# Optimization experiments

Hardware: AMD Instinct MI355X
Metric: run time of the kernel (lower is better)

Reference implementation:

```python
import jax, jax.numpy as jnp
import numpy as np

B, N, D = 64, 784, 768
H, HD, G = 32, 24, 2
HID = 3072
SCALE = HD ** -0.5
EPS = 1e-6


def _ln(x, g, b):
    m = jnp.mean(x, -1, keepdims=True)
    v = jnp.mean((x - m) ** 2, -1, keepdims=True)
    return (x - m) * jax.lax.rsqrt(v + EPS) * g + b


def setup_inputs() -> dict:
    key = jax.random.key(0)
    ks = jax.random.split(key, 12)
    def rn(k, shape, s=0.02):
        return (jax.random.normal(k, shape) * s).astype(jnp.float32)
    return {
        'x_cls': jax.random.normal(ks[0], (B, 1, D), jnp.float32),
        'x_img': jax.random.normal(ks[1], (B, N, D), jnp.float32),
        'ln1_g': jnp.ones((D,), jnp.float32), 'ln1_b': jnp.zeros((D,), jnp.float32),
        'Wq': rn(ks[2], (D, D)), 'bq': jnp.zeros((D,), jnp.float32),
        'Wk': rn(ks[3], (D, D)), 'bk': jnp.zeros((D,), jnp.float32),
        'Wv': rn(ks[4], (D, D)), 'bv': jnp.zeros((D,), jnp.float32),
        'w1_W': rn(ks[5], (H, H), 0.1), 'w1_b': jnp.zeros((H,), jnp.float32),
        'w2_W': rn(ks[6], (H, H), 0.1), 'w2_b': jnp.zeros((H,), jnp.float32),
        'proj_W': rn(ks[7], (D, D)), 'proj_b': jnp.zeros((D,), jnp.float32),
        'ln2_g': jnp.ones((D,), jnp.float32), 'ln2_b': jnp.zeros((D,), jnp.float32),
        'fc1_W': rn(ks[8], (G, HID // G, D // G)), 'fc1_b': jnp.zeros((G, HID // G), jnp.float32),
        'fc2_W': rn(ks[9], (G, D // G, HID // G)), 'fc2_b': jnp.zeros((G, D // G), jnp.float32),
    }


def reference(x_cls, x_img, ln1_g, ln1_b, Wq, bq, Wk, bk, Wv, bv,
              w1_W, w1_b, w2_W, w2_b, proj_W, proj_b, ln2_g, ln2_b,
              fc1_W, fc1_b, fc2_W, fc2_b):
    # --- ClassAttention (non-mismatch path), dropout = identity (eval) ---
    u = jnp.concatenate([x_cls, x_img], axis=1)  # [B, M, D], M = N+1
    M = u.shape[1]
    n = _ln(u, ln1_g, ln1_b)
    q = ((n[:, :1] @ Wq + bq).reshape(B, 1, H, HD).transpose(0, 2, 1, 3)) * SCALE  # [B,H,1,HD]
    k = (n @ Wk + bk).reshape(B, M, H, HD).transpose(0, 2, 1, 3)                   # [B,H,M,HD]
    v = (n @ Wv + bv).reshape(B, M, H, HD).transpose(0, 2, 1, 3)
    attn = jnp.einsum('bhqd,bhkd->bhqk', q, k)  # [B,H,1,M]
    # interactive score mixing across heads (w1 pre-softmax, w2 post-softmax)
    attn = attn + jnp.einsum('bhqk,hg->bgqk', attn, w1_W) + w1_b[None, :, None, None]
    attn = jax.nn.softmax(attn, axis=-1)
    attn = attn + jnp.einsum('bhqk,hg->bgqk', attn, w2_W) + w2_b[None, :, None, None]
    o = jnp.einsum('bhqk,bhkd->bhqd', attn, v).transpose(0, 2, 1, 3).reshape(B, 1, D)
    x_cls = x_cls + (o @ proj_W + proj_b)
    # --- GroupConvMlp on the cls token (grouped 1x1 convs + channel shuffle) ---
    y = _ln(x_cls, ln2_g, ln2_b)
    h = jnp.einsum('btgc,goc->btgo', y.reshape(B, 1, G, D // G), fc1_W) + fc1_b  # group-major out channels
    h = jax.nn.gelu(h.reshape(B, 1, HID), approximate=False)
    # channel_shuffle(group=G): out channel b*gc+a = in channel a*G+b
    h = h.reshape(B, 1, HID // G, G).transpose(0, 1, 3, 2).reshape(B, 1, HID)
    z = jnp.einsum('btgc,goc->btgo', h.reshape(B, 1, G, HID // G), fc2_W) + fc2_b
    x_cls = x_cls + z.reshape(B, 1, D)
    return (x_cls, x_img)
```

## Files before the change

### kernel.cpp

```cpp
#include <hip/hip_runtime.h>
#include <hip/hip_bf16.h>
#include <math.h>

#define BB   64
#define NN   784
#define DD   768
#define HH   32
#define HD24 24
#define MM   785
#define HIDN 3072
#define QSCALE 0.20412414523193154f
#define LNEPS 1e-6f

#define WS_Q     0
#define WS_RS    49152
#define WS_RM    100352
#define WS_S1P   151552
#define WS_BQP   163840
#define WS_LMX   176128
#define WS_LSM   184320
#define WS_A2P   192512
#define WS_WMP   200704
#define WS_PS    208896
#define WS_C1    210432
#define WS_H2    259584
#define WS_O     456192
#define WS_E     505344
#define WS_T     2143744
#define WS_ZP    0

__device__ __forceinline__ unsigned packbf(float a, float b) {
  union { __hip_bfloat162 h2; unsigned u; } cv;
  cv.h2 = __float22bfloat162_rn(make_float2(a, b));
  return cv.u;
}
__device__ __forceinline__ float lo16(unsigned w) { return __uint_as_float(w << 16); }
__device__ __forceinline__ float hi16(unsigned w) { return __uint_as_float(w & 0xffff0000u); }

__global__ __launch_bounds__(256) void k_q(
    const float* __restrict__ x_cls,
    const float* __restrict__ g1, const float* __restrict__ b1,
    const float* __restrict__ Wq, const float* __restrict__ bq,
    float* __restrict__ ws)
{
  const int b = blockIdx.y;
  const int oc0 = blockIdx.x * 64;
  const int t = threadIdx.x;
  const int lane = t & 63, wid = t >> 6;

  __shared__ __align__(16) float nc_l[DD];
  __shared__ float red4[4][64];
  __shared__ float rS[4], rQ[4];
  __shared__ float musd[2];

  float xv[3];
  float s = 0.f, q2 = 0.f;
#pragma unroll
  for (int k = 0; k < 3; ++k) {
    float v = x_cls[(size_t)b * DD + t + 256 * k];
    xv[k] = v; s += v; q2 += v * v;
  }
#pragma unroll
  for (int off = 1; off < 64; off <<= 1) { s += __shfl_xor(s, off); q2 += __shfl_xor(q2, off); }
  if (lane == 0) { rS[wid] = s; rQ[wid] = q2; }
  __syncthreads();
  if (t == 0) {
    float ss = rS[0] + rS[1] + rS[2] + rS[3];
    float qq = rQ[0] + rQ[1] + rQ[2] + rQ[3];
    float mu = ss * (1.f / DD);
    musd[0] = mu; musd[1] = rsqrtf(qq * (1.f / DD) - mu * mu + LNEPS);
  }
  __syncthreads();
  {
    float mu = musd[0], rs = musd[1];
#pragma unroll
    for (int k = 0; k < 3; ++k) {
      int d = t + 256 * k;
      nc_l[d] = (xv[k] - mu) * rs * g1[d] + b1[d];
    }
  }
  __syncthreads();

  const int oc = t & 63, ks = t >> 6;
  const float* wp = Wq + (size_t)(ks * 192) * DD + oc0 + oc;
  const float* ncp = nc_l + ks * 192;
  float a0 = 0.f, a1 = 0.f, a2 = 0.f, a3 = 0.f;
#pragma unroll 4
  for (int d = 0; d < 192; d += 4) {
    a0 += ncp[d + 0] * wp[(size_t)(d + 0) * DD];
    a1 += ncp[d + 1] * wp[(size_t)(d + 1) * DD];
    a2 += ncp[d + 2] * wp[(size_t)(d + 2) * DD];
    a3 += ncp[d + 3] * wp[(size_t)(d + 3) * DD];
  }
  red4[ks][oc] = (a0 + a1) + (a2 + a3);
  __syncthreads();
  if (t < 64) {
    int ocg = oc0 + t;
    ws[WS_Q + (size_t)b * DD + ocg] =
        (red4[0][t] + red4[1][t] + red4[2][t] + red4[3][t] + bq[ocg]) * QSCALE;
  }
}

__global__ __launch_bounds__(256) void k_gqk(
    const float* __restrict__ g1, const float* __restrict__ b1,
    const float* __restrict__ Wk, const float* __restrict__ w1W,
    float* __restrict__ ws)
{
  const int b = blockIdx.y;
  const int d0 = blockIdx.x * 128;
  const int t = threadIdx.x;

  __shared__ __align__(16) float q_l[DD];
  __shared__ float T1[HH * HH];
  __shared__ float qk_l[128][33];
  __shared__ float pS[8][HH], pB[8][HH];

  for (int i = t; i < DD; i += 256) q_l[i] = ws[WS_Q + (size_t)b * DD + i];
  for (int i = t; i < HH * HH; i += 256) {
    int g = i >> 5, h = i & 31;
    T1[i] = w1W[i] + ((g == h) ? 1.f : 0.f);
  }
  __syncthreads();

  {
    const int dl = t >> 1, gh = t & 1;
    const float4* wr = (const float4*)(Wk + (size_t)(d0 + dl) * DD + gh * 384);
    const float4* qr = (const float4*)(q_l + gh * 384);
#pragma unroll 4
    for (int gg = 0; gg < 16; ++gg) {
      float a = 0.f;
#pragma unroll
      for (int c = 0; c < 6; ++c) {
        float4 w = wr[gg * 6 + c];
        float4 p = qr[gg * 6 + c];
        a += w.x * p.x + w.y * p.y + w.z * p.z + w.w * p.w;
      }
      qk_l[dl][gh * 16 + gg] = a;
    }
  }
  __syncthreads();
  {
    const int h = t & 31, dg = t >> 5;
    float fb[16];
    float s1a = 0.f, bqa = 0.f;
#pragma unroll 2
    for (int dd = 0; dd < 16; ++dd) {
      int dl = dg * 16 + dd;
      float f = 0.f;
#pragma unroll 8
      for (int g = 0; g < HH; ++g) f += qk_l[dl][g] * T1[g * HH + h];
      float gq = g1[d0 + dl] * f;
      fb[dd] = gq;
      s1a += gq;
      bqa += b1[d0 + dl] * qk_l[dl][h];
    }
    float* gout = ws + WS_E + ((size_t)b * HH + h) * DD + d0 + dg * 16;
#pragma unroll
    for (int k = 0; k < 4; ++k)
      *(float4*)(gout + k * 4) = make_float4(fb[4*k], fb[4*k+1], fb[4*k+2], fb[4*k+3]);
    pS[dg][h] = s1a; pB[dg][h] = bqa;
  }
  __syncthreads();
  if (t < HH) {
    float s = 0.f, bq = 0.f;
#pragma unroll
    for (int k = 0; k < 8; ++k) { s += pS[k][t]; bq += pB[k][t]; }
    ws[WS_S1P + ((size_t)b * 6 + blockIdx.x) * HH + t] = s;
    ws[WS_BQP + ((size_t)b * 6 + blockIdx.x) * HH + t] = bq;
  }
}

__global__ __launch_bounds__(256) void k_main1(
    const float* __restrict__ x_cls, const float* __restrict__ x_img,
    float* __restrict__ out, float* __restrict__ ws)
{
  const int b = blockIdx.y;
  const int m0 = blockIdx.x * 64;
  const int t = threadIdx.x;
  const int rp = t >> 3;
  const int pc = (t & 7) * 4;
  const int mo = t & 7;
  const int dsub = (t >> 3) & 7;
  const int th = t >> 6;

  __shared__ unsigned uT[32][36];
  __shared__ __align__(16) float gqT[32][36];

  const float* gq_src = ws + WS_E + (size_t)b * (HH * DD);
  float* out_img = out + (size_t)BB * DD;

  const int ma = m0 + 2 * rp;
  const int mb = ma + 1;
  const bool va = (ma < MM), vb = (mb < MM);
  const float* rowA = (ma == 0) ? (x_cls + (size_t)b * DD)
                                : (x_img + ((size_t)b * NN + (ma - 1)) * DD);
  const float* rowB = x_img + ((size_t)b * NN + (mb - 1)) * DD;
  float* orowA = out_img + ((size_t)b * NN + (ma - 1)) * DD;
  float* orowB = out_img + ((size_t)b * NN + (mb - 1)) * DD;

  float4 pf0, pf1, pfg;
  float sl0 = 0.f, sq0 = 0.f, sl1 = 0.f, sq1 = 0.f;

  auto LOADX = [&](int dc) {
    pf0 = va ? *(const float4*)(rowA + dc * 32 + pc) : make_float4(0.f,0.f,0.f,0.f);
    pf1 = vb ? *(const float4*)(rowB + dc * 32 + pc) : make_float4(0.f,0.f,0.f,0.f);
    sl0 += pf0.x + pf0.y + pf0.z + pf0.w;
    sq0 += pf0.x*pf0.x + pf0.y*pf0.y + pf0.z*pf0.z + pf0.w*pf0.w;
    sl1 += pf1.x + pf1.y + pf1.z + pf1.w;
    sq1 += pf1.x*pf1.x + pf1.y*pf1.y + pf1.z*pf1.z + pf1.w*pf1.w;
    pfg = *(const float4*)(gq_src + (size_t)rp * DD + dc * 32 + pc);
  };
  auto STOREX = [&](int dc) {
    if (va && ma >= 1) *(float4*)(orowA + dc * 32 + pc) = pf0;
    if (vb)            *(float4*)(orowB + dc * 32 + pc) = pf1;
    uT[pc + 0][rp] = packbf(pf0.x, pf1.x);
    uT[pc + 1][rp] = packbf(pf0.y, pf1.y);
    uT[pc + 2][rp] = packbf(pf0.z, pf1.z);
    uT[pc + 3][rp] = packbf(pf0.w, pf1.w);
    *(float4*)&gqT[rp][pc] = pfg;
  };

  float acc[8][8];
#pragma unroll
  for (int i = 0; i < 8; ++i)
#pragma unroll
    for (int j = 0; j < 8; ++j) acc[i][j] = 0.f;

  LOADX(0); STOREX(0); __syncthreads();

#define K1_DD2(COMP, DD2LIT)                                            \
  {                                                                     \
    uint4 uw = *(const uint4*)&uT[dsub * 4 + DD2LIT][mo * 4];           \
    float um0 = lo16(uw.x), um1 = hi16(uw.x);                           \
    float um2 = lo16(uw.y), um3 = hi16(uw.y);                           \
    float um4 = lo16(uw.z), um5 = hi16(uw.z);                           \
    float um6 = lo16(uw.w), um7 = hi16(uw.w);                           \
    _Pragma("unroll")                                                   \
    for (int j = 0; j < 8; ++j) {                                       \
      const float g = gq4[j].COMP;                                      \
      acc[0][j] += um0 * g; acc[1][j] += um1 * g;                       \
      acc[2][j] += um2 * g; acc[3][j] += um3 * g;                       \
      acc[4][j] += um4 * g; acc[5][j] += um5 * g;                       \
      acc[6][j] += um6 * g; acc[7][j] += um7 * g;                       \
    }                                                                   \
  }

  for (int dc = 0; dc < 24; ++dc) {
    if (dc < 23) LOADX(dc + 1);
    float4 gq4[8];
#pragma unroll
    for (int j = 0; j < 8; ++j) gq4[j] = *(const float4*)&gqT[th * 8 + j][dsub * 4];
    K1_DD2(x, 0)
    K1_DD2(y, 1)
    K1_DD2(z, 2)
    K1_DD2(w, 3)
    __syncthreads();
    if (dc < 23) STOREX(dc + 1);
    __syncthreads();
  }
#undef K1_DD2

#pragma unroll
  for (int i = 0; i < 8; ++i)
#pragma unroll
    for (int j = 0; j < 8; ++j) {
      float v = acc[i][j];
      v += __shfl_xor(v, 8);
      v += __shfl_xor(v, 16);
      v += __shfl_xor(v, 32);
      acc[i][j] = v;
    }
  if (dsub == 0) {
    float* tb = ws + WS_T + (size_t)b * MM * HH;
#pragma unroll
    for (int i = 0; i < 8; ++i) {
      int m = m0 + mo * 8 + i;
      if (m < MM) {
        float* dst = tb + (size_t)m * HH + th * 8;
        *(float4*)dst = make_float4(acc[i][0], acc[i][1], acc[i][2], acc[i][3]);
        *(float4*)(dst + 4) = make_float4(acc[i][4], acc[i][5], acc[i][6], acc[i][7]);
      }
    }
  }
#pragma unroll
  for (int off = 1; off < 8; off <<= 1) {
    sl0 += __shfl_xor(sl0, off); sq0 += __shfl_xor(sq0, off);
    sl1 += __shfl_xor(sl1, off); sq1 += __shfl_xor(sq1, off);
  }
  if ((t & 7) == 0) {
    if (va) {
      float mu = sl0 * (1.f / DD);
      float rs = rsqrtf(sq0 * (1.f / DD) - mu * mu + LNEPS);
      ws[WS_RS + (size_t)b * 800 + ma] = rs;
      ws[WS_RM + (size_t)b * 800 + ma] = rs * mu;
    }
    if (vb) {
      float mu = sl1 * (1.f / DD);
      float rs = rsqrtf(sq1 * (1.f / DD) - mu * mu + LNEPS);
      ws[WS_RS + (size_t)b * 800 + mb] = rs;
      ws[WS_RM + (size_t)b * 800 + mb] = rs * mu;
    }
  }
}

__global__ __launch_bounds__(256) void k_sm_a(
    const float* __restrict__ bk,
    const float* __restrict__ w1W, const float* __restrict__ w1b,
    float* __restrict__ ws)
{
  const int cx = blockIdx.x, b = blockIdx.y;
  const int t = threadIdx.x;
  const int lane = t & 63, wid = t >> 6;

  __shared__ float T1[HH * HH];
  __shared__ float s1_sh[HH], c0_sh[HH], bq_sh[HH];
  __shared__ float red[4][HH];
  __shared__ float lmax_sh[HH];

  for (int i = t; i < HH * HH; i += 256) {
    int g = i >> 5, h = i & 31;
    T1[i] = w1W[i] + ((g == h) ? 1.f : 0.f);
  }
  if (t < HH) {
    float s1v = 0.f, bqv = 0.f;
#pragma unroll
    for (int p = 0; p < 6; ++p) {
      s1v += ws[WS_S1P + ((size_t)b * 6 + p) * HH + t];
      bqv += ws[WS_BQP + ((size_t)b * 6 + p) * HH + t];
    }
    const float* qp = ws + WS_Q + (size_t)b * DD + t * HD24;
#pragma unroll
    for (int j = 0; j < HD24; ++j) bqv += bk[t * HD24 + j] * qp[j];
    s1_sh[t] = s1v; bq_sh[t] = bqv;
  }
  __syncthreads();
  if (t < HH) {
    float c0 = w1b[t];
#pragma unroll
    for (int g = 0; g < HH; ++g) c0 += T1[g * HH + t] * bq_sh[g];
    c0_sh[t] = c0;
  }
  __syncthreads();

  const int m = cx * 256 + t;
  const bool vm = (m < MM);
  float a1[HH];
  if (vm) {
    const float* tb = ws + WS_T + ((size_t)b * MM + m) * HH;
    float rs = ws[WS_RS + (size_t)b * 800 + m];
    float rm = ws[WS_RM + (size_t)b * 800 + m];
#pragma unroll
    for (int q = 0; q < 8; ++q) {
      float4 tv = *(const float4*)(tb + q * 4);
      a1[4*q+0] = rs * tv.x - rm * s1_sh[4*q+0] + c0_sh[4*q+0];
      a1[4*q+1] = rs * tv.y - rm * s1_sh[4*q+1] + c0_sh[4*q+1];
      a1[4*q+2] = rs * tv.z - rm * s1_sh[4*q+2] + c0_sh[4*q+2];
      a1[4*q+3] = rs * tv.w - rm * s1_sh[4*q+3] + c0_sh[4*q+3];
    }
  } else {
#pragma unroll
    for (int h = 0; h < HH; ++h) a1[h] = -3.0e38f;
  }
#pragma unroll
  for (int h = 0; h < HH; ++h) {
    float v = a1[h];
#pragma unroll
    for (int off = 1; off < 64; off <<= 1) v = fmaxf(v, __shfl_xor(v, off));
    if (lane == 0) red[wid][h] = v;
  }
  __syncthreads();
  if (t < HH) {
    float v = fmaxf(fmaxf(red[0][t], red[1][t]), fmaxf(red[2][t], red[3][t]));
    lmax_sh[t] = v;
    ws[WS_LMX + ((size_t)b * 4 + cx) * HH + t] = v;
  }
  __syncthreads();
  float* E = ws + WS_E + (size_t)b * (HH * 800);
  if (vm) {
#pragma unroll
    for (int h = 0; h < HH; ++h) {
      float e = __expf(a1[h] - lmax_sh[h]);
      a1[h] = e;
      E[(size_t)h * 800 + m] = e;
    }
  } else {
#pragma unroll
    for (int h = 0; h < HH; ++h) a1[h] = 0.f;
  }
#pragma unroll
  for (int h = 0; h < HH; ++h) {
    float v = a1[h];
#pragma unroll
    for (int off = 1; off < 64; off <<= 1) v += __shfl_xor(v, off);
    if (lane == 0) red[wid][h] = v;
  }
  __syncthreads();
  if (t < HH)
    ws[WS_LSM + ((size_t)b * 4 + cx) * HH + t] = red[0][t] + red[1][t] + red[2][t] + red[3][t];
}

__global__ __launch_bounds__(256) void k_sm_b(
    const float* __restrict__ w2W, const float* __restrict__ w2b,
    float* __restrict__ ws)
{
  const int cx = blockIdx.x, b = blockIdx.y;
  const int t = threadIdx.x;
  const int lane = t & 63, wid = t >> 6;

  __shared__ __align__(16) float T2s[HH * HH];
  __shared__ float inv_sh[HH], w2b_sh[HH];
  __shared__ float red[4][HH];

  if (t < HH) {
    float l0 = ws[WS_LMX + ((size_t)b * 4 + 0) * HH + t];
    float l1 = ws[WS_LMX + ((size_t)b * 4 + 1) * HH + t];
    float l2 = ws[WS_LMX + ((size_t)b * 4 + 2) * HH + t];
    float l3 = ws[WS_LMX + ((size_t)b * 4 + 3) * HH + t];
    float gmax = fmaxf(fmaxf(l0, l1), fmaxf(l2, l3));
    float s = ws[WS_LSM + ((size_t)b * 4 + 0) * HH + t] * __expf(l0 - gmax)
            + ws[WS_LSM + ((size_t)b * 4 + 1) * HH + t] * __expf(l1 - gmax)
            + ws[WS_LSM + ((size_t)b * 4 + 2) * HH + t] * __expf(l2 - gmax)
            + ws[WS_LSM + ((size_t)b * 4 + 3) * HH + t] * __expf(l3 - gmax);
    float lcx = (cx == 0) ? l0 : (cx == 1) ? l1 : (cx == 2) ? l2 : l3;
    inv_sh[t] = __expf(lcx - gmax) / s;
    w2b_sh[t] = w2b[t];
  }
  __syncthreads();
  for (int i = t; i < HH * HH; i += 256) {
    int g = i >> 5, h = i & 31;
    T2s[i] = (w2W[i] + ((g == h) ? 1.f : 0.f)) * inv_sh[g];
  }
  __syncthreads();

  const int m = cx * 256 + t;
  float* E = ws + WS_E + (size_t)b * (HH * 800);
  float4 av[8];
#pragma unroll
  for (int q = 0; q < 8; ++q) av[q] = make_float4(0.f,0.f,0.f,0.f);
  float rm = 0.f;
  if (m < MM) {
    float rs = ws[WS_RS + (size_t)b * 800 + m];
    rm = ws[WS_RM + (size_t)b * 800 + m];
#pragma unroll 4
    for (int g = 0; g < HH; ++g) {
      float eg = E[(size_t)g * 800 + m];
#pragma unroll
      for (int q = 0; q < 8; ++q) {
        float4 t2 = *(const float4*)&T2s[g * HH + q * 4];
        av[q].x += eg * t2.x; av[q].y += eg * t2.y;
        av[q].z += eg * t2.z; av[q].w += eg * t2.w;
      }
    }
#pragma unroll
    for (int q = 0; q < 8; ++q) {
      av[q].x += w2b_sh[q*4+0]; av[q].y += w2b_sh[q*4+1];
      av[q].z += w2b_sh[q*4+2]; av[q].w += w2b_sh[q*4+3];
      E[(size_t)(q*4+0) * 800 + m] = av[q].x * rs;
      E[(size_t)(q*4+1) * 800 + m] = av[q].y * rs;
      E[(size_t)(q*4+2) * 800 + m] = av[q].z * rs;
      E[(size_t)(q*4+3) * 800 + m] = av[q].w * rs;
    }
  } else if (m < 800) {
#pragma unroll
    for (int h = 0; h < HH; ++h) E[(size_t)h * 800 + m] = 0.f;
  }
#pragma unroll
  for (int h = 0; h < HH; ++h) {
    float v = ((const float*)&av[h >> 2])[h & 3];
#pragma unroll
    for (int off = 1; off < 64; off <<= 1) v += __shfl_xor(v, off);
    if (lane == 0) red[wid][h] = v;
  }
  __syncthreads();
  if (t < HH)
    ws[WS_A2P + ((size_t)b * 4 + cx) * HH + t] = red[0][t] + red[1][t] + red[2][t] + red[3][t];
  __syncthreads();
#pragma unroll
  for (int h = 0; h < HH; ++h) {
    float v = ((const float*)&av[h >> 2])[h & 3] * rm;
#pragma unroll
    for (int off = 1; off < 64; off <<= 1) v += __shfl_xor(v, off);
    if (lane == 0) red[wid][h] = v;
  }
  __syncthreads();
  if (t < HH)
    ws[WS_WMP + ((size_t)b * 4 + cx) * HH + t] = red[0][t] + red[1][t] + red[2][t] + red[3][t];
}

__global__ __launch_bounds__(256) void k_wsum(
    const float* __restrict__ x_cls, const float* __restrict__ x_img,
    float* __restrict__ ws)
{
  const int b = blockIdx.y;
  const int d0 = blockIdx.x * 64;
  const int t = threadIdx.x;
  const int dseg = t & 15;
  const int msub = (t >> 4) & 3;
  const int hb = (t >> 6) * 8;

  __shared__ __align__(16) float w_s[HH][36];
  const float* W = ws + WS_E + (size_t)b * (HH * 800);

  float acc[8][4];
#pragma unroll
  for (int j = 0; j < 8; ++j)
#pragma unroll
    for (int c = 0; c < 4; ++c) acc[j][c] = 0.f;

  float4 pu[8], pun[8];
  float4 pwn;

  auto LOADU = [&](int mc, float4* dst) {
#pragma unroll
    for (int i = 0; i < 8; ++i) {
      int m = mc * 32 + msub * 8 + i;
      if (m < MM) {
        const float* src = (m == 0) ? (x_cls + (size_t)b * DD)
                                    : (x_img + ((size_t)b * NN + (m - 1)) * DD);
        dst[i] = *(const float4*)(src + d0 + dseg * 4);
      } else dst[i] = make_float4(0.f,0.f,0.f,0.f);
    }
  };

  LOADU(0, pu);
  {
    float4 pw = *(const float4*)(W + (size_t)(t >> 3) * 800 + (t & 7) * 4);
    *(float4*)&w_s[t >> 3][(t & 7) * 4] = pw;
  }
  __syncthreads();

  for (int mc = 0; mc < 25; ++mc) {
    if (mc < 24) {
      pwn = *(const float4*)(W + (size_t)(t >> 3) * 800 + (mc + 1) * 32 + (t & 7) * 4);
      LOADU(mc + 1, pun);
    }
#pragma unroll
    for (int j = 0; j < 8; ++j) {
      float4 wA = *(const float4*)&w_s[hb + j][msub * 8];
      float4 wB = *(const float4*)&w_s[hb + j][msub * 8 + 4];
      float wv0 = wA.x, wv1 = wA.y, wv2 = wA.z, wv3 = wA.w;
      float wv4 = wB.x, wv5 = wB.y, wv6 = wB.z, wv7 = wB.w;
      acc[j][0] += wv0*pu[0].x + wv1*pu[1].x + wv2*pu[2].x + wv3*pu[3].x
                 + wv4*pu[4].x + wv5*pu[5].x + wv6*pu[6].x + wv7*pu[7].x;
      acc[j][1] += wv0*pu[0].y + wv1*pu[1].y + wv2*pu[2].y + wv3*pu[3].y
                 + wv4*pu[4].y + wv5*pu[5].y + wv6*pu[6].y + wv7*pu[7].y;
      acc[j][2] += wv0*pu[0].z + wv1*pu[1].z + wv2*pu[2].z + wv3*pu[3].z
                 + wv4*pu[4].z + wv5*pu[5].z + wv6*pu[6].z + wv7*pu[7].z;
      acc[j][3] += wv0*pu[0].w + wv1*pu[1].w + wv2*pu[2].w + wv3*pu[3].w
                 + wv4*pu[4].w + wv5*pu[5].w + wv6*pu[6].w + wv7*pu[7].w;
    }
    __syncthreads();
    if (mc < 24) {
      *(float4*)&w_s[t >> 3][(t & 7) * 4] = pwn;
#pragma unroll
      for (int i = 0; i < 8; ++i) pu[i] = pun[i];
    }
    __syncthreads();
  }

#pragma unroll
  for (int j = 0; j < 8; ++j)
#pragma unroll
    for (int c = 0; c < 4; ++c) {
      float v = acc[j][c];
      v += __shfl_xor(v, 16);
      v += __shfl_xor(v, 32);
      acc[j][c] = v;
    }
  if (msub == 0) {
    float* R = ws + WS_T + (size_t)b * HH * DD;
#pragma unroll
    for (int j = 0; j < 8; ++j)
      *(float4*)(R + (size_t)(hb + j) * DD + d0 + dseg * 4) =
          make_float4(acc[j][0], acc[j][1], acc[j][2], acc[j][3]);
  }
}

__global__ __launch_bounds__(192) void k_att_o(
    const float* __restrict__ g1, const float* __restrict__ b1,
    const float* __restrict__ Wv, const float* __restrict__ bv,
    float* __restrict__ ws)
{
  const int h = blockIdx.x;
  const int b = blockIdx.y;
  const int t = threadIdx.x;

  __shared__ __align__(16) float agg_l[DD];
  __shared__ float red[8][25];
  __shared__ float a2wm[2];

  if (t == 0) {
    float a = 0.f;
#pragma unroll
    for (int c = 0; c < 4; ++c) a += ws[WS_A2P + ((size_t)b * 4 + c) * HH + h];
    a2wm[0] = a;
  }
  if (t == 1) {
    float w = 0.f;
#pragma unroll
    for (int c = 0; c < 4; ++c) w += ws[WS_WMP + ((size_t)b * 4 + c) * HH + h];
    a2wm[1] = w;
  }
  __syncthreads();
  const float A2 = a2wm[0], WM = a2wm[1];
  const float* R = ws + WS_T + ((size_t)b * HH + h) * DD;
  for (int i = t; i < DD; i += 192)
    agg_l[i] = g1[i] * (R[i] - WM) + b1[i] * A2;
  __syncthreads();

  const int oc = t % 24, ks = t / 24;
  const float* wv = Wv + (size_t)(ks * 96) * DD + h * HD24 + oc;
  const float* ag = agg_l + ks * 96;
  float a0 = 0.f, a1 = 0.f, a2 = 0.f, a3 = 0.f;
#pragma unroll 4
  for (int d = 0; d < 96; d += 4) {
    a0 += ag[d + 0] * wv[(size_t)(d + 0) * DD];
    a1 += ag[d + 1] * wv[(size_t)(d + 1) * DD];
    a2 += ag[d + 2] * wv[(size_t)(d + 2) * DD];
    a3 += ag[d + 3] * wv[(size_t)(d + 3) * DD];
  }
  red[ks][oc] = (a0 + a1) + (a2 + a3);
  __syncthreads();
  if (t < 24) {
    float o = A2 * bv[h * HD24 + t];
#pragma unroll
    for (int k = 0; k < 8; ++k) o += red[k][t];
    ws[WS_O + (size_t)b * DD + h * HD24 + t] = o;
  }
}

__global__ __launch_bounds__(256) void k_proj2(
    const float* __restrict__ x_cls,
    const float* __restrict__ projW, const float* __restrict__ projb,
    float* __restrict__ ws)
{
  const int b = blockIdx.y;
  const int oc0 = blockIdx.x * 64;
  const int t = threadIdx.x;

  __shared__ __align__(16) float o_l[DD];
  __shared__ float red4[4][64];

  for (int i = t; i < DD; i += 256) o_l[i] = ws[WS_O + (size_t)b * DD + i];
  __syncthreads();

  const int oc = t & 63, ks = t >> 6;
  const float* wp = projW + (size_t)(ks * 192) * DD + oc0 + oc;
  const float* op = o_l + ks * 192;
  float a0 = 0.f, a1 = 0.f, a2 = 0.f, a3 = 0.f;
#pragma unroll 4
  for (int d = 0; d < 192; d += 4) {
    a0 += op[d + 0] * wp[(size_t)(d + 0) * DD];
    a1 += op[d + 1] * wp[(size_t)(d + 1) * DD];
    a2 += op[d + 2] * wp[(size_t)(d + 2) * DD];
    a3 += op[d + 3] * wp[(size_t)(d + 3) * DD];
  }
  red4[ks][oc] = (a0 + a1) + (a2 + a3);
  __syncthreads();
  if (t < 64) {
    int ocg = oc0 + t;
    float c1 = red4[0][t] + red4[1][t] + red4[2][t] + red4[3][t]
             + projb[ocg] + x_cls[(size_t)b * DD + ocg];
    ws[WS_C1 + (size_t)b * DD + ocg] = c1;
    float cs = c1, cq = c1 * c1;
#pragma unroll
    for (int off = 1; off < 64; off <<= 1) { cs += __shfl_xor(cs, off); cq += __shfl_xor(cq, off); }
    if (t == 0) {
      ws[WS_PS + ((size_t)b * 12 + blockIdx.x) * 2 + 0] = cs;
      ws[WS_PS + ((size_t)b * 12 + blockIdx.x) * 2 + 1] = cq;
    }
  }
}

__global__ __launch_bounds__(256) void k_fc1(
    const float* __restrict__ fc1W, const float* __restrict__ fc1b,
    const float* __restrict__ g2, const float* __restrict__ b2,
    float* __restrict__ ws)
{
  const int g = blockIdx.x / 48;
  const int oc0 = (blockIdx.x % 48) * 32;
  const int t = threadIdx.x;
  const int txo = t & 7, tyb = t >> 3;

  __shared__ float y_s[64][65];
  __shared__ float w_s[32][65];
  __shared__ float mv[64][2];

  if (t < 64) {
    float s = 0.f, q = 0.f;
#pragma unroll
    for (int p = 0; p < 12; ++p) {
      s += ws[WS_PS + ((size_t)t * 12 + p) * 2 + 0];
      q += ws[WS_PS + ((size_t)t * 12 + p) * 2 + 1];
    }
    float mu = s * (1.f / DD);
    mv[t][0] = mu;
    mv[t][1] = rsqrtf(q * (1.f / DD) - mu * mu + LNEPS);
  }
  __syncthreads();

  float acc[2][4];
#pragma unroll
  for (int i = 0; i < 2; ++i)
#pragma unroll
    for (int j = 0; j < 4; ++j) acc[i][j] = 0.f;

#pragma unroll 1
  for (int kc = 0; kc < 6; ++kc) {
    {
      int r = t >> 2;
      float mu = mv[r][0], rs = mv[r][1];
#pragma unroll
      for (int p = 0; p < 4; ++p) {
        int c = (t & 3) * 4 + p * 16;
        int gc = g * 384 + kc * 64 + c;
        float4 v = *(const float4*)(ws + WS_C1 + (size_t)r * DD + gc);
        float4 gg = *(const float4*)(g2 + gc);
        float4 bb = *(const float4*)(b2 + gc);
        y_s[r][c+0] = (v.x - mu) * rs * gg.x + bb.x;
        y_s[r][c+1] = (v.y - mu) * rs * gg.y + bb.y;
        y_s[r][c+2] = (v.z - mu) * rs * gg.z + bb.z;
        y_s[r][c+3] = (v.w - mu) * rs * gg.w + bb.w;
      }
      int rw = t >> 3;
#pragma unroll
      for (int p = 0; p < 2; ++p) {
        int c = (t & 7) * 4 + p * 32;
        float4 w = *(const float4*)(fc1W + ((size_t)(g * 1536 + oc0 + rw)) * 384 + kc * 64 + c);
        w_s[rw][c+0] = w.x; w_s[rw][c+1] = w.y; w_s[rw][c+2] = w.z; w_s[rw][c+3] = w.w;
      }
    }
    __syncthreads();
#pragma unroll 4
    for (int kk = 0; kk < 64; ++kk) {
      float y0 = y_s[2*tyb+0][kk], y1 = y_s[2*tyb+1][kk];
      float w0 = w_s[4*txo+0][kk], w1 = w_s[4*txo+1][kk];
      float w2 = w_s[4*txo+2][kk], w3 = w_s[4*txo+3][kk];
      acc[0][0] += y0*w0; acc[0][1] += y0*w1; acc[0][2] += y0*w2; acc[0][3] += y0*w3;
      acc[1][0] += y1*w0; acc[1][1] += y1*w1; acc[1][2] += y1*w2; acc[1][3] += y1*w3;
    }
    __syncthreads();
  }

  float* H2 = ws + WS_H2;
#pragma unroll
  for (int i = 0; i < 2; ++i) {
    int bb = 2 * tyb + i;
#pragma unroll
    for (int j = 0; j < 4; ++j) {
      int oc = oc0 + 4 * txo + j;
      float v = acc[i][j] + fc1b[g * 1536 + oc];
      v = 0.5f * v * (1.f + erff(v * 0.70710678118654752f));
      H2[(size_t)bb * HIDN + (oc & 1) * 1536 + g * 768 + (oc >> 1)] = v;
    }
  }
}

__global__ __launch_bounds__(256) void k_fc2(
    const float* __restrict__ fc2W, float* __restrict__ ws)
{
  const int oc0 = blockIdx.x * 32;
  const int kq = blockIdx.y;
  const int g = blockIdx.z;
  const int t = threadIdx.x;
  const int txo = t & 7, tyb = t >> 3;

  __shared__ float h_s[64][65];
  __shared__ float w_s[32][65];

  float acc[2][4];
#pragma unroll
  for (int i = 0; i < 2; ++i)
#pragma unroll
    for (int j = 0; j < 4; ++j) acc[i][j] = 0.f;

  const float* H2 = ws + WS_H2;

#pragma unroll 1
  for (int kc = 0; kc < 6; ++kc) {
    {
      int r = t >> 2;
#pragma unroll
      for (int p = 0; p < 4; ++p) {
        int c = (t & 3) * 4 + p * 16;
        float4 v = *(const float4*)(H2 + (size_t)r * HIDN + g * 1536 + kq * 384 + kc * 64 + c);
        h_s[r][c+0] = v.x; h_s[r][c+1] = v.y; h_s[r][c+2] = v.z; h_s[r][c+3] = v.w;
      }
      int rw = t >> 3;
#pragma unroll
      for (int p = 0; p < 2; ++p) {
        int c = (t & 7) * 4 + p * 32;
        float4 w = *(const float4*)(fc2W + ((size_t)(g * 384 + oc0 + rw)) * 1536 + kq * 384 + kc * 64 + c);
        w_s[rw][c+0] = w.x; w_s[rw][c+1] = w.y; w_s[rw][c+2] = w.z; w_s[rw][c+3] = w.w;
      }
    }
    __syncthreads();
#pragma unroll 4
    for (int kk = 0; kk < 64; ++kk) {
      float y0 = h_s[2*tyb+0][kk], y1 = h_s[2*tyb+1][kk];
      float w0 = w_s[4*txo+0][kk], w1 = w_s[4*txo+1][kk];
      float w2 = w_s[4*txo+2][kk], w3 = w_s[4*txo+3][kk];
      acc[0][0] += y0*w0; acc[0][1] += y0*w1; acc[0][2] += y0*w2; acc[0][3] += y0*w3;
      acc[1][0] += y1*w0; acc[1][1] += y1*w1; acc[1][2] += y1*w2; acc[1][3] += y1*w3;
    }
    __syncthreads();
  }

  float* ZP = ws + WS_ZP + (size_t)kq * BB * DD;
#pragma unroll
  for (int i = 0; i < 2; ++i)
#pragma unroll
    for (int j = 0; j < 4; ++j)
      ZP[(size_t)(2 * tyb + i) * DD + g * 384 + oc0 + 4 * txo + j] = acc[i][j];
}

__global__ __launch_bounds__(256) void k_final(
    const float* __restrict__ fc2b, float* __restrict__ out, const float* __restrict__ ws)
{
  int idx = blockIdx.x * 256 + threadIdx.x;
  int d = idx % DD;
  float v = ws[WS_C1 + idx] + fc2b[d];
#pragma unroll
  for (int kq = 0; kq < 4; ++kq) v += ws[WS_ZP + (size_t)kq * BB * DD + idx];
  out[idx] = v;
}

extern "C" void kernel_launch(void* const* d_in, const int* in_sizes, int n_in,
                              void* d_out, int out_size, void* d_ws, size_t ws_size,
                              hipStream_t stream)
{
  (void)in_sizes; (void)n_in; (void)out_size; (void)ws_size;
  const float* x_cls = (const float*)d_in[0];
  const float* x_img = (const float*)d_in[1];
  const float* ln1_g = (const float*)d_in[2];
  const float* ln1_b = (const float*)d_in[3];
  const float* Wq    = (const float*)d_in[4];
  const float* bq    = (const float*)d_in[5];
  const float* Wk    = (const float*)d_in[6];
  const float* bk    = (const float*)d_in[7];
  const float* Wv    = (const float*)d_in[8];
  const float* bv    = (const float*)d_in[9];
  const float* w1W   = (const float*)d_in[10];
  const float* w1b   = (const float*)d_in[11];
  const float* w2W   = (const float*)d_in[12];
  const float* w2b   = (const float*)d_in[13];
  const float* projW = (const float*)d_in[14];
  const float* projb = (const float*)d_in[15];
  const float* ln2_g = (const float*)d_in[16];
  const float* ln2_b = (const float*)d_in[17];
  const float* fc1W  = (const float*)d_in[18];
  const float* fc1b  = (const float*)d_in[19];
  const float* fc2W  = (const float*)d_in[20];
  const float* fc2b  = (const float*)d_in[21];
  float* out = (float*)d_out;
  float* ws  = (float*)d_ws;

  k_q    <<<dim3(12, 64), dim3(256), 0, stream>>>(x_cls, ln1_g, ln1_b, Wq, bq, ws);
  k_gqk  <<<dim3(6, 64),  dim3(256), 0, stream>>>(ln1_g, ln1_b, Wk, w1W, ws);
  k_main1<<<dim3(13, 64), dim3(256), 0, stream>>>(x_cls, x_img, out, ws);
  k_sm_a <<<dim3(4, 64),  dim3(256), 0, stream>>>(bk, w1W, w1b, ws);
  k_sm_b <<<dim3(4, 64),  dim3(256), 0, stream>>>(w2W, w2b, ws);
  k_wsum <<<dim3(12, 64), dim3(256), 0, stream>>>(x_cls, x_img, ws);
  k_att_o<<<dim3(32, 64), dim3(192), 0, stream>>>(ln1_g, ln1_b, Wv, bv, ws);
  k_proj2<<<dim3(12, 64), dim3(256), 0, stream>>>(x_cls, projW, projb, ws);
  k_fc1  <<<dim3(96),     dim3(256), 0, stream>>>(fc1W, fc1b, ln2_g, ln2_b, ws);
  k_fc2  <<<dim3(12, 4, 2), dim3(256), 0, stream>>>(fc2W, ws);
  k_final<<<dim3(192),    dim3(256), 0, stream>>>(fc2b, out, ws);
}
```

Before: 335.7 us.

## Use bf16 MFMA for the x·gq score projection with pre-swizzled B operand

The producer kernel now writes the gq matrix as bf16 in the MFMA B-operand lane layout, and k_main1 replaces its scalar FMA outer-product loop and LDS staging with 16x16x32 bf16 MFMA instructions. A-operand rows are read directly from global memory per lane, while the x_img-to-output copy is done in a separate coalesced loop. This is meant to remove the VALU-bound inner product and the shared-memory transposes and barriers. The cost is that each input row is read twice from global memory (once for the copy, once for the A operand), the gq values drop to bf16, and the A-operand reads are less coalesced.

Result: faster. 320.4 us (-4.6%).

```diff
diff --git a/kernel.cpp b/kernel.cpp
--- a/kernel.cpp
+++ b/kernel.cpp
@@ -29,6 +29,9 @@
 #define WS_T     2143744
 #define WS_ZP    0
 
+typedef __attribute__((ext_vector_type(8))) short bf16x8;
+typedef __attribute__((ext_vector_type(4))) float f32x4;
+
 __device__ __forceinline__ unsigned packbf(float a, float b) {
   union { __hip_bfloat162 h2; unsigned u; } cv;
   cv.h2 = __float22bfloat162_rn(make_float2(a, b));
@@ -154,10 +157,16 @@
       s1a += gq;
       bqa += b1[d0 + dl] * qk_l[dl][h];
     }
-    float* gout = ws + WS_E + ((size_t)b * HH + h) * DD + d0 + dg * 16;
-#pragma unroll
-    for (int k = 0; k < 4; ++k)
-      *(float4*)(gout + k * 4) = make_float4(fb[4*k], fb[4*k+1], fb[4*k+2], fb[4*k+3]);
+    const int kstep = (d0 >> 5) + (dg >> 1);
+    const int nt = h >> 4;
+    const int lane0 = (h & 15) + 32 * (dg & 1);
+    uint4* GQB = (uint4*)(ws + WS_E) + (size_t)b * (24 * 2 * 64);
+    GQB[(kstep * 2 + nt) * 64 + lane0] =
+        make_uint4(packbf(fb[0], fb[1]), packbf(fb[2], fb[3]),
+                   packbf(fb[4], fb[5]), packbf(fb[6], fb[7]));
+    GQB[(kstep * 2 + nt) * 64 + lane0 + 16] =
+        make_uint4(packbf(fb[8], fb[9]), packbf(fb[10], fb[11]),
+                   packbf(fb[12], fb[13]), packbf(fb[14], fb[15]));
     pS[dg][h] = s1a; pB[dg][h] = bqa;
   }
   __syncthreads();
@@ -177,128 +186,78 @@
   const int b = blockIdx.y;
   const int m0 = blockIdx.x * 64;
   const int t = threadIdx.x;
-  const int rp = t >> 3;
-  const int pc = (t & 7) * 4;
-  const int mo = t & 7;
-  const int dsub = (t >> 3) & 7;
-  const int th = t >> 6;
-
-  __shared__ unsigned uT[32][36];
-  __shared__ __align__(16) float gqT[32][36];
-
-  const float* gq_src = ws + WS_E + (size_t)b * (HH * DD);
+  const int w = t >> 6;
+  const int l = t & 63;
+  const int lg = l >> 4;
+  const int lm = l & 15;
+
+  const uint4* GQ = (const uint4*)(ws + WS_E) + (size_t)b * (24 * 2 * 64);
   float* out_img = out + (size_t)BB * DD;
 
-  const int ma = m0 + 2 * rp;
-  const int mb = ma + 1;
-  const bool va = (ma < MM), vb = (mb < MM);
-  const float* rowA = (ma == 0) ? (x_cls + (size_t)b * DD)
-                                : (x_img + ((size_t)b * NN + (ma - 1)) * DD);
-  const float* rowB = x_img + ((size_t)b * NN + (mb - 1)) * DD;
-  float* orowA = out_img + ((size_t)b * NN + (ma - 1)) * DD;
-  float* orowB = out_img + ((size_t)b * NN + (mb - 1)) * DD;
-
-  float4 pf0, pf1, pfg;
-  float sl0 = 0.f, sq0 = 0.f, sl1 = 0.f, sq1 = 0.f;
-
-  auto LOADX = [&](int dc) {
-    pf0 = va ? *(const float4*)(rowA + dc * 32 + pc) : make_float4(0.f,0.f,0.f,0.f);
-    pf1 = vb ? *(const float4*)(rowB + dc * 32 + pc) : make_float4(0.f,0.f,0.f,0.f);
-    sl0 += pf0.x + pf0.y + pf0.z + pf0.w;
-    sq0 += pf0.x*pf0.x + pf0.y*pf0.y + pf0.z*pf0.z + pf0.w*pf0.w;
-    sl1 += pf1.x + pf1.y + pf1.z + pf1.w;
-    sq1 += pf1.x*pf1.x + pf1.y*pf1.y + pf1.z*pf1.z + pf1.w*pf1.w;
-    pfg = *(const float4*)(gq_src + (size_t)rp * DD + dc * 32 + pc);
-  };
-  auto STOREX = [&](int dc) {
-    if (va && ma >= 1) *(float4*)(orowA + dc * 32 + pc) = pf0;
-    if (vb)            *(float4*)(orowB + dc * 32 + pc) = pf1;
-    uT[pc + 0][rp] = packbf(pf0.x, pf1.x);
-    uT[pc + 1][rp] = packbf(pf0.y, pf1.y);
-    uT[pc + 2][rp] = packbf(pf0.z, pf1.z);
-    uT[pc + 3][rp] = packbf(pf0.w, pf1.w);
-    *(float4*)&gqT[rp][pc] = pfg;
-  };
-
-  float acc[8][8];
-#pragma unroll
-  for (int i = 0; i < 8; ++i)
-#pragma unroll
-    for (int j = 0; j < 8; ++j) acc[i][j] = 0.f;
-
-  LOADX(0); STOREX(0); __syncthreads();
-
-#define K1_DD2(COMP, DD2LIT)                                            \
-  {                                                                     \
-    uint4 uw = *(const uint4*)&uT[dsub * 4 + DD2LIT][mo * 4];           \
-    float um0 = lo16(uw.x), um1 = hi16(uw.x);                           \
-    float um2 = lo16(uw.y), um3 = hi16(uw.y);                           \
-    float um4 = lo16(uw.z), um5 = hi16(uw.z);                           \
-    float um6 = lo16(uw.w), um7 = hi16(uw.w);                           \
-    _Pragma("unroll")                                                   \
-    for (int j = 0; j < 8; ++j) {                                       \
-      const float g = gq4[j].COMP;                                      \
-      acc[0][j] += um0 * g; acc[1][j] += um1 * g;                       \
-      acc[2][j] += um2 * g; acc[3][j] += um3 * g;                       \
-      acc[4][j] += um4 * g; acc[5][j] += um5 * g;                       \
-      acc[6][j] += um6 * g; acc[7][j] += um7 * g;                       \
-    }                                                                   \
-  }
-
-  for (int dc = 0; dc < 24; ++dc) {
-    if (dc < 23) LOADX(dc + 1);
-    float4 gq4[8];
-#pragma unroll
-    for (int j = 0; j < 8; ++j) gq4[j] = *(const float4*)&gqT[th * 8 + j][dsub * 4];
-    K1_DD2(x, 0)
-    K1_DD2(y, 1)
-    K1_DD2(z, 2)
-    K1_DD2(w, 3)
-    __syncthreads();
-    if (dc < 23) STOREX(dc + 1);
-    __syncthreads();
-  }
-#undef K1_DD2
-
-#pragma unroll
-  for (int i = 0; i < 8; ++i)
-#pragma unroll
-    for (int j = 0; j < 8; ++j) {
-      float v = acc[i][j];
-      v += __shfl_xor(v, 8);
-      v += __shfl_xor(v, 16);
-      v += __shfl_xor(v, 32);
-      acc[i][j] = v;
-    }
-  if (dsub == 0) {
-    float* tb = ws + WS_T + (size_t)b * MM * HH;
-#pragma unroll
-    for (int i = 0; i < 8; ++i) {
-      int m = m0 + mo * 8 + i;
-      if (m < MM) {
-        float* dst = tb + (size_t)m * HH + th * 8;
-        *(float4*)dst = make_float4(acc[i][0], acc[i][1], acc[i][2], acc[i][3]);
-        *(float4*)(dst + 4) = make_float4(acc[i][4], acc[i][5], acc[i][6], acc[i][7]);
+  const int arow = m0 + w * 16 + lm;
+  const bool av = (arow < MM);
+  const int arc = av ? arow : 0;
+  const float* asrc = (arc == 0) ? (x_cls + (size_t)b * DD)
+                                 : (x_img + ((size_t)b * NN + (arc - 1)) * DD);
+  const int koff_l = 8 * lg;
+
+  f32x4 acc0 = {0.f, 0.f, 0.f, 0.f};
+  f32x4 acc1 = {0.f, 0.f, 0.f, 0.f};
+  float sl = 0.f, sq = 0.f;
+
+#pragma unroll 1
+  for (int kc = 0; kc < 12; ++kc) {
+#pragma unroll
+    for (int p = 0; p < 4; ++p) {
+      int i = p * 256 + t;
+      int crow = m0 + (i >> 4);
+      int cc = i & 15;
+      if (crow < MM) {
+        const float* src = (crow == 0) ? (x_cls + (size_t)b * DD)
+                                       : (x_img + ((size_t)b * NN + (crow - 1)) * DD);
+        float4 v = *(const float4*)(src + kc * 64 + cc * 4);
+        if (crow >= 1)
+          *(float4*)(out_img + ((size_t)b * NN + (crow - 1)) * DD + kc * 64 + cc * 4) = v;
       }
     }
-  }
-#pragma unroll
-  for (int off = 1; off < 8; off <<= 1) {
-    sl0 += __shfl_xor(sl0, off); sq0 += __shfl_xor(sq0, off);
-    sl1 += __shfl_xor(sl1, off); sq1 += __shfl_xor(sq1, off);
-  }
-  if ((t & 7) == 0) {
-    if (va) {
-      float mu = sl0 * (1.f / DD);
-      float rs = rsqrtf(sq0 * (1.f / DD) - mu * mu + LNEPS);
-      ws[WS_RS + (size_t)b * 800 + ma] = rs;
-      ws[WS_RM + (size_t)b * 800 + ma] = rs * mu;
-    }
-    if (vb) {
-      float mu = sl1 * (1.f / DD);
-      float rs = rsqrtf(sq1 * (1.f / DD) - mu * mu + LNEPS);
-      ws[WS_RS + (size_t)b * 800 + mb] = rs;
-      ws[WS_RM + (size_t)b * 800 + mb] = rs * mu;
+#pragma unroll
+    for (int s = 0; s < 2; ++s) {
+      const int kst = kc * 2 + s;
+      float4 a0 = make_float4(0.f, 0.f, 0.f, 0.f);
+      float4 a1 = make_float4(0.f, 0.f, 0.f, 0.f);
+      if (av) {
+        a0 = *(const float4*)(asrc + kst * 32 + koff_l);
+        a1 = *(const float4*)(asrc + kst * 32 + koff_l + 4);
+      }
+      sl += (a0.x + a0.y) + (a0.z + a0.w) + (a1.x + a1.y) + (a1.z + a1.w);
+      sq += a0.x*a0.x + a0.y*a0.y + a0.z*a0.z + a0.w*a0.w
+          + a1.x*a1.x + a1.y*a1.y + a1.z*a1.z + a1.w*a1.w;
+      union { uint4 u; bf16x8 h; } ua, ub0, ub1;
+      ua.u = make_uint4(packbf(a0.x, a0.y), packbf(a0.z, a0.w),
+                        packbf(a1.x, a1.y), packbf(a1.z, a1.w));
+      ub0.u = GQ[(kst * 2 + 0) * 64 + l];
+      ub1.u = GQ[(kst * 2 + 1) * 64 + l];
+      acc0 = __builtin_amdgcn_mfma_f32_16x16x32_bf16(ua.h, ub0.h, acc0, 0, 0, 0);
+      acc1 = __builtin_amdgcn_mfma_f32_16x16x32_bf16(ua.h, ub1.h, acc1, 0, 0, 0);
+    }
+  }
+
+  sl += __shfl_xor(sl, 16); sl += __shfl_xor(sl, 32);
+  sq += __shfl_xor(sq, 16); sq += __shfl_xor(sq, 32);
+  if (lg == 0 && av) {
+    float mu = sl * (1.f / DD);
+    float rs = rsqrtf(sq * (1.f / DD) - mu * mu + LNEPS);
+    ws[WS_RS + (size_t)b * 800 + arow] = rs;
+    ws[WS_RM + (size_t)b * 800 + arow] = rs * mu;
+  }
+
+  float* tb = ws + WS_T + (size_t)b * MM * HH;
+#pragma unroll
+  for (int r = 0; r < 4; ++r) {
+    int row = m0 + w * 16 + 4 * lg + r;
+    if (row < MM) {
+      tb[(size_t)row * HH + lm] = acc0[r];
+      tb[(size_t)row * HH + 16 + lm] = acc1[r];
     }
   }
 }
```
